# Kernel optimization log

Hardware: AMD Instinct MI355X
Metric: run time of the kernel (lower is better)

The kernel has to match this reference:

```python
import jax, jax.numpy as jnp
import numpy as np
import math

B, T, O, C, H, L, V, S = 4, 1024, 128, 1024, 16, 4, 32000, 4096
D = C // H
PAD = 0


def setup_inputs() -> dict:
    key = jax.random.key(0)
    ks = jax.random.split(key, 16)
    r = lambda i, shape, s=0.02: jax.random.normal(ks[i], shape, jnp.float32) * s
    return {
        "tokens_w": jax.random.randint(ks[0], (B, T), 0, V).astype(jnp.int32),
        "pos_offset": 0,
        "mem": jax.random.normal(ks[1], (B, O, C), jnp.float32),
        "ssum": jax.random.normal(ks[2], (B, C), jnp.float32),
        "tok_emb_w": r(3, (V, C)),
        "pos_emb_w": r(4, (S, C)),
        "mem_w": r(5, (C, C)), "mem_b": jnp.zeros((C,), jnp.float32),
        "memln_s": jnp.ones((C,), jnp.float32), "memln_b": jnp.zeros((C,), jnp.float32),
        "alpha_p": jnp.zeros((C,), jnp.float32),
        "sum_w": r(6, (C, C)),
        "ln1_s": jnp.ones((L, C), jnp.float32), "ln1_b": jnp.zeros((L, C), jnp.float32),
        "Wq": r(7, (L, C, C)), "bq": jnp.zeros((L, C), jnp.float32),
        "Wk": r(8, (L, C, C)), "bk": jnp.zeros((L, C), jnp.float32),
        "Wv": r(9, (L, C, C)), "bv": jnp.zeros((L, C), jnp.float32),
        "Wo": r(10, (L, C, C)), "bo": jnp.zeros((L, C), jnp.float32),
        "ln2_s": jnp.ones((L, C), jnp.float32), "ln2_b": jnp.zeros((L, C), jnp.float32),
        "W1": r(11, (L, C, 4 * C)), "b1": jnp.zeros((L, 4 * C), jnp.float32),
        "W2": r(12, (L, 4 * C, C)), "b2": jnp.zeros((L, C), jnp.float32),
        "fln_s": jnp.ones((C,), jnp.float32), "fln_b": jnp.zeros((C,), jnp.float32),
        "head_w": r(13, (C, V)), "head_b": jnp.zeros((V,), jnp.float32),
        "lam_p": jnp.zeros((C,), jnp.float32),
    }


def _ln(x, s, b, eps=1e-6):
    mu = jnp.mean(x, -1, keepdims=True)
    var = jnp.mean((x - mu) ** 2, -1, keepdims=True)
    return (x - mu) * jax.lax.rsqrt(var + eps) * s + b


def reference(tokens_w, pos_offset, mem, ssum, tok_emb_w, pos_emb_w, mem_w, mem_b,
              memln_s, memln_b, alpha_p, sum_w, ln1_s, ln1_b, Wq, bq, Wk, bk, Wv, bv,
              Wo, bo, ln2_s, ln2_b, W1, b1, W2, b2, fln_s, fln_b, head_w, head_b, lam_p):
    Bx, Tx = tokens_w.shape
    tok = tok_emb_w[tokens_w]                                   # [B,T,C]
    pos_ids = jnp.clip(jnp.arange(Tx, dtype=jnp.int32) + pos_offset, 0, S - 1)
    x = tok + pos_emb_w[pos_ids][None, :, :]
    # memory adapter + norm (saved-before-masking memory state)
    m2 = _ln(mem @ mem_w + mem_b, memln_s, memln_b)             # [B,O,C]
    alpha = jax.nn.sigmoid(alpha_p)
    x = x + ((ssum @ sum_w) * alpha[None, :])[:, None, :]
    # boolean mask: memory tokens always visible + causal window + key padding
    causal = jnp.concatenate([jnp.ones((Tx, O), bool),
                              jnp.tril(jnp.ones((Tx, Tx), bool))], axis=1)[None, None]
    key_ok = jnp.concatenate([jnp.ones((Bx, O), bool), tokens_w != PAD], axis=1)
    mask = causal & key_ok[:, None, None, :]                    # [B,1,T,O+T]
    scale = 1.0 / math.sqrt(D)
    for i in range(L):
        kv = jnp.concatenate([m2, x], axis=1)                   # [B,O+T,C]
        h = _ln(x, ln1_s[i], ln1_b[i])
        q = (h @ Wq[i] + bq[i]).reshape(Bx, Tx, H, D)
        k = (kv @ Wk[i] + bk[i]).reshape(Bx, O + Tx, H, D)
        v = (kv @ Wv[i] + bv[i]).reshape(Bx, O + Tx, H, D)
        att = jnp.einsum('bqhd,bkhd->bhqk', q, k) * scale
        att = jnp.where(mask, att, -1e9)
        p = jax.nn.softmax(att, axis=-1)
        o = jnp.einsum('bhqk,bkhd->bqhd', p, v).reshape(Bx, Tx, C)
        x = x + (o @ Wo[i] + bo[i])
        h = _ln(x, ln2_s[i], ln2_b[i])
        x = x + (jax.nn.gelu(h @ W1[i] + b1[i]) @ W2[i] + b2[i])
    x = _ln(x, fln_s, fln_b)
    new_mem = x[:, -O:, :]
    m = (tokens_w != PAD).astype(x.dtype)
    x = x * m[:, :, None]
    logits = x @ head_w + head_b                                # [B,T,V]
    summary = jnp.sum(x * m[:, :, None], axis=1) / (jnp.sum(m, axis=1, keepdims=True) + 1e-6)
    lam = jax.nn.sigmoid(lam_p)
    new_ssum = ssum * lam[None, :] + summary * (1.0 - lam[None, :])
    return (new_mem, new_ssum, logits)
```

## Files before the change

kernel.cpp:

```cpp
#include <hip/hip_runtime.h>
#include <hip/hip_bf16.h>

typedef __bf16 bf16_t;
typedef __bf16 bf16x8 __attribute__((ext_vector_type(8)));
typedef __bf16 bf16x4 __attribute__((ext_vector_type(4)));
typedef float f32x4 __attribute__((ext_vector_type(4)));

#define NB 4
#define NT 1024
#define NO 128
#define NC 1024
#define NH 16
#define NL 4
#define NV 32000
#define NS 4096
#define ND 64
#define NTK (NO + NT)

#define GLOAD_LDS16(g, l) __builtin_amdgcn_global_load_lds( \
    (__attribute__((address_space(1))) void*)(g), \
    (__attribute__((address_space(3))) void*)(l), 16, 0, 0)

__device__ __forceinline__ float sigmoidf_(float x) { return 1.0f / (1.0f + __expf(-x)); }

#define EPI_F32  0
#define EPI_ADD  1
#define EPI_GELU 2
#define EPI_QKV  3
#define EPI_KV   4

template<int EPI>
__global__ __launch_bounds__(512) void gemm8p(
    const bf16_t* __restrict__ A, const bf16_t* __restrict__ Bt,
    const float* __restrict__ bias, float* __restrict__ outF,
    bf16_t* __restrict__ outB, int M, int N, int K, int ldo, int gm)
{
    __shared__ bf16_t sm[65536];
    const int tid = threadIdx.x;
    const int w = tid >> 6, lane = tid & 63;
    const int wr = w >> 2, wc = w & 3;
    const int lr = lane & 15, lk = lane >> 4;
    const int nwg = gridDim.x;
    const int bid = blockIdx.x;
    const int xcd = bid & 7, base = bid >> 3;
    const int qq = nwg >> 3, rr = nwg & 7;
    int wg = (xcd < rr ? xcd * (qq + 1) : rr * (qq + 1) + (xcd - rr) * qq) + base;
    const int nnt = N >> 8;
    const int gsz = gm * nnt;
    const int g = wg / gsz, r2 = wg - g * gsz;
    const int ntl = r2 / gm, mt = g * gm + (r2 - ntl * gm);
    const int bm = mt << 8, bn = ntl << 8;
    const bf16_t* Ab = A + (size_t)bm * K;
    const bf16_t* Bb = Bt + (size_t)bn * K;
    const int srow = tid >> 3;
    const int scol = ((tid & 7) ^ (srow & 7)) << 3;
    const int nk = K >> 6;
    f32x4 acc[8][4] = {};

    auto STAGE = [&](int b, int kt, int h) {
        const bf16_t* gsrc = (h < 2) ? Ab : Bb;
        const int half = h & 1;
        char* lbase = (char*)(sm + ((h < 2) ? 0 : 32768) + b * 16384 + half * 8192);
        #pragma unroll
        for (int i = 0; i < 2; ++i) {
            GLOAD_LDS16(gsrc + (size_t)(half * 128 + i * 64 + srow) * K + kt * 64 + scol,
                        lbase + (i * 512 + tid) * 16);
        }
    };

    #pragma unroll
    for (int h = 0; h < 4; ++h) STAGE(0, 0, h);
    asm volatile("s_waitcnt vmcnt(0)" ::: "memory");
    __builtin_amdgcn_s_barrier();

    for (int kt = 0; kt < nk; ++kt) {
        const int curb = kt & 1;
        const bool dostage = (kt + 1) < nk;
        const char* Abase = (const char*)(sm + curb * 16384);
        const char* Bbase = (const char*)(sm + 32768 + curb * 16384);

        if (dostage) {
            STAGE(curb ^ 1, kt + 1, 0);
            STAGE(curb ^ 1, kt + 1, 1);
            asm volatile("s_waitcnt vmcnt(4)" ::: "memory");
        } else {
            asm volatile("s_waitcnt vmcnt(0)" ::: "memory");
        }
        __builtin_amdgcn_s_barrier();

        bf16x8 bfr[4][2];
        #pragma unroll
        for (int n = 0; n < 4; ++n)
            #pragma unroll
            for (int ks = 0; ks < 2; ++ks) {
                const int row = wc * 64 + n * 16 + lr;
                bfr[n][ks] = *(const bf16x8*)(Bbase + row * 128 + ((((ks << 2) + lk) ^ (row & 7)) << 4));
            }
        bf16x8 af[4][2];
        #pragma unroll
        for (int m = 0; m < 4; ++m)
            #pragma unroll
            for (int ks = 0; ks < 2; ++ks) {
                const int row = wr * 128 + m * 16 + lr;
                af[m][ks] = *(const bf16x8*)(Abase + row * 128 + ((((ks << 2) + lk) ^ (row & 7)) << 4));
            }
        asm volatile("s_waitcnt lgkmcnt(0)" ::: "memory");
        __builtin_amdgcn_sched_barrier(0);
        __builtin_amdgcn_s_setprio(1);
        #pragma unroll
        for (int m = 0; m < 4; ++m)
            #pragma unroll
            for (int n = 0; n < 4; ++n)
                #pragma unroll
                for (int ks = 0; ks < 2; ++ks)
                    acc[m][n] = __builtin_amdgcn_mfma_f32_16x16x32_bf16(
                        af[m][ks], bfr[n][ks], acc[m][n], 0, 0, 0);
        __builtin_amdgcn_s_setprio(0);

        if (dostage) {
            STAGE(curb ^ 1, kt + 1, 2);
            STAGE(curb ^ 1, kt + 1, 3);
        }
        bf16x8 ag[4][2];
        #pragma unroll
        for (int m = 0; m < 4; ++m)
            #pragma unroll
            for (int ks = 0; ks < 2; ++ks) {
                const int row = wr * 128 + 64 + m * 16 + lr;
                ag[m][ks] = *(const bf16x8*)(Abase + row * 128 + ((((ks << 2) + lk) ^ (row & 7)) << 4));
            }
        asm volatile("s_waitcnt lgkmcnt(0)" ::: "memory");
        __builtin_amdgcn_sched_barrier(0);
        __builtin_amdgcn_s_setprio(1);
        #pragma unroll
        for (int m = 0; m < 4; ++m)
            #pragma unroll
            for (int n = 0; n < 4; ++n)
                #pragma unroll
                for (int ks = 0; ks < 2; ++ks)
                    acc[4 + m][n] = __builtin_amdgcn_mfma_f32_16x16x32_bf16(
                        ag[m][ks], bfr[n][ks], acc[4 + m][n], 0, 0, 0);
        __builtin_amdgcn_s_setprio(0);
        __builtin_amdgcn_s_barrier();
    }

    float bv4[4];
    #pragma unroll
    for (int n = 0; n < 4; ++n) bv4[n] = bias[bn + wc * 64 + n * 16 + lr];
    #pragma unroll
    for (int m = 0; m < 8; ++m) {
        #pragma unroll
        for (int j = 0; j < 4; ++j) {
            const int row = bm + wr * 128 + m * 16 + lk * 4 + j;
            #pragma unroll
            for (int n = 0; n < 4; ++n) {
                const int col = bn + wc * 64 + n * 16 + lr;
                float v = acc[m][n][j] + bv4[n];
                if constexpr (EPI == 0) {
                    __builtin_nontemporal_store(v, &outF[(size_t)row * ldo + col]);
                } else {
                    float u = 1.5957691216057308f * (v + 0.044715f * v * v * v);
                    float g_ = v / (1.0f + __expf(-u));
                    outB[(size_t)row * ldo + col] = (bf16_t)g_;
                }
            }
        }
    }
}

template<int EPI>
__global__ __launch_bounds__(256) void gemm128(
    const bf16_t* __restrict__ A, const bf16_t* __restrict__ Bt,
    const float* __restrict__ bias, const float* __restrict__ bias2,
    float* __restrict__ outF, bf16_t* __restrict__ outB, bf16_t* __restrict__ outB2,
    int M, int N, int K, int p0, int ldo, int gm)
{
    __shared__ bf16_t sm[32768];
    char* smb = (char*)sm;
    const int tid = threadIdx.x;
    const int w = tid >> 6, lane = tid & 63;
    const int wr = w >> 1, wc = w & 1;
    const int lr = lane & 15, lk = lane >> 4;
    const int nwg = gridDim.x;
    const int bid = blockIdx.x;
    const int xcd = bid & 7, base = bid >> 3;
    const int qq = nwg >> 3, rr = nwg & 7;
    int wg = (xcd < rr ? xcd * (qq + 1) : rr * (qq + 1) + (xcd - rr) * qq) + base;
    const int nnt = N >> 7;
    const int gsz = gm * nnt;
    const int g = wg / gsz, r2 = wg - g * gsz;
    const int ntl = r2 / gm, mt = g * gm + (r2 - ntl * gm);
    const int bm = mt << 7, bn = ntl << 7;
    const bf16_t* Ab = A + (size_t)bm * K;
    const bf16_t* Bb = Bt + (size_t)bn * K;
    const int srow = tid >> 3;
    const int scol = ((tid & 7) ^ (srow & 7)) << 3;
    const int nk = K >> 6;
    f32x4 acc[4][4] = {};

    auto STAGE = [&](int b, int kt, int h) {
        const bf16_t* gsrc = h ? Bb : Ab;
        char* lbase = smb + h * 32768 + b * 16384;
        #pragma unroll
        for (int i = 0; i < 4; ++i) {
            GLOAD_LDS16(gsrc + (size_t)(i * 32 + srow) * K + kt * 64 + scol,
                        lbase + (i * 256 + tid) * 16);
        }
    };

    STAGE(0, 0, 0); STAGE(0, 0, 1);
    asm volatile("s_waitcnt vmcnt(0)" ::: "memory");
    __builtin_amdgcn_s_barrier();

    for (int kt = 0; kt < nk; ++kt) {
        const int curb = kt & 1;
        const bool dostage = (kt + 1) < nk;
        const char* Abase = smb + curb * 16384;
        const char* Bbase = smb + 32768 + curb * 16384;

        if (dostage) {
            STAGE(curb ^ 1, kt + 1, 0);
            asm volatile("s_waitcnt vmcnt(4)" ::: "memory");
        } else {
            asm volatile("s_waitcnt vmcnt(0)" ::: "memory");
        }
        __builtin_amdgcn_s_barrier();

        bf16x8 bfr[4][2];
        #pragma unroll
        for (int n = 0; n < 4; ++n)
            #pragma unroll
            for (int ks = 0; ks < 2; ++ks) {
                const int row = wc * 64 + n * 16 + lr;
                bfr[n][ks] = *(const bf16x8*)(Bbase + row * 128 + ((((ks << 2) + lk) ^ (row & 7)) << 4));
            }
        bf16x8 af[4];
        #pragma unroll
        for (int m = 0; m < 4; ++m) {
            const int row = wr * 64 + m * 16 + lr;
            af[m] = *(const bf16x8*)(Abase + row * 128 + (((lk) ^ (row & 7)) << 4));
        }
        asm volatile("s_waitcnt lgkmcnt(0)" ::: "memory");
        __builtin_amdgcn_sched_barrier(0);
        __builtin_amdgcn_s_setprio(1);
        #pragma unroll
        for (int m = 0; m < 4; ++m)
            #pragma unroll
            for (int n = 0; n < 4; ++n)
                acc[m][n] = __builtin_amdgcn_mfma_f32_16x16x32_bf16(
                    af[m], bfr[n][0], acc[m][n], 0, 0, 0);
        __builtin_amdgcn_s_setprio(0);

        if (dostage) STAGE(curb ^ 1, kt + 1, 1);
        bf16x8 ag[4];
        #pragma unroll
        for (int m = 0; m < 4; ++m) {
            const int row = wr * 64 + m * 16 + lr;
            ag[m] = *(const bf16x8*)(Abase + row * 128 + (((4 + lk) ^ (row & 7)) << 4));
        }
        asm volatile("s_waitcnt lgkmcnt(0)" ::: "memory");
        __builtin_amdgcn_sched_barrier(0);
        __builtin_amdgcn_s_setprio(1);
        #pragma unroll
        for (int m = 0; m < 4; ++m)
            #pragma unroll
            for (int n = 0; n < 4; ++n)
                acc[m][n] = __builtin_amdgcn_mfma_f32_16x16x32_bf16(
                    ag[m], bfr[n][1], acc[m][n], 0, 0, 0);
        __builtin_amdgcn_s_setprio(0);
        __builtin_amdgcn_s_barrier();
    }

    #pragma unroll
    for (int m = 0; m < 4; ++m) {
        #pragma unroll
        for (int j = 0; j < 4; ++j) {
            const int row = bm + wr * 64 + m * 16 + lk * 4 + j;
            int b_ = 0, t_ = 0;
            if constexpr (EPI == EPI_QKV || EPI == EPI_KV) { b_ = row / p0; t_ = row % p0; }
            #pragma unroll
            for (int n = 0; n < 4; ++n) {
                const int col = bn + wc * 64 + n * 16 + lr;
                if constexpr (EPI == EPI_F32) {
                    float v = acc[m][n][j] + bias[col];
                    __builtin_nontemporal_store(v, &outF[(size_t)row * ldo + col]);
                } else if constexpr (EPI == EPI_ADD) {
                    float v = acc[m][n][j] + bias[col];
                    outF[(size_t)row * ldo + col] += v;
                } else if constexpr (EPI == EPI_QKV) {
                    float v = acc[m][n][j] + bias[col];
                    int h = col >> 6, d = col & 63;
                    outB[(((size_t)b_ * NH + h) * p0 + t_) * ND + d] = (bf16_t)v;
                } else if constexpr (EPI == EPI_KV) {
                    if (col < NC) {
                        float v = acc[m][n][j] + bias[col];
                        int h = col >> 6, d = col & 63;
                        outB[(((size_t)b_ * NH + h) * NTK + t_) * ND + d] = (bf16_t)v;
                    } else {
                        int c2_ = col - NC;
                        float v = acc[m][n][j] + bias2[c2_];
                        int h = c2_ >> 6, d = c2_ & 63;
                        outB2[(((size_t)b_ * NH + h) * ND + d) * NTK + t_] = (bf16_t)v;
                    }
                }
            }
        }
    }
}

template<int EPI>
__global__ __launch_bounds__(256) void gemm_bt(
    const bf16_t* __restrict__ A, const bf16_t* __restrict__ Bt,
    const float* __restrict__ bias, const float* __restrict__ bias2,
    float* __restrict__ outF, bf16_t* __restrict__ outB, bf16_t* __restrict__ outB2,
    int M, int N, int K, int p0, int ldo, int gm)
{
    __shared__ bf16_t lA[128 * 32];
    __shared__ bf16_t lB[128 * 32];
    const int tid = threadIdx.x;
    const int nwg = gridDim.x;
    const int bid = blockIdx.x;
    const int xcd = bid & 7, base = bid >> 3;
    const int qq = nwg >> 3, rr = nwg & 7;
    int wg = (xcd < rr ? xcd * (qq + 1) : rr * (qq + 1) + (xcd - rr) * qq) + base;
    const int nnt = N >> 7;
    const int gsz = gm * nnt;
    const int g = wg / gsz, r2 = wg - g * gsz;
    const int ntl = r2 / gm, mt = g * gm + (r2 - ntl * gm);
    const int bm = mt * 128, bn = ntl * 128;
    const bf16_t* Ab = A + (size_t)bm * K;
    const bf16_t* Bb = Bt + (size_t)bn * K;
    const int wave = tid >> 6, lane = tid & 63;
    const int wr = wave >> 1, wc = wave & 1;
    const int lr = lane & 15, lk = lane >> 4;
    f32x4 acc[4][4] = {};
    const int nk = K >> 5;
    const int c1 = tid, c2 = tid + 256;
    for (int kt = 0; kt < nk; ++kt) {
        __syncthreads();
        const bf16_t* Abk = Ab + kt * 32;
        const bf16_t* Bbk = Bb + kt * 32;
        GLOAD_LDS16(Abk + (size_t)(c1 >> 2) * K + (c1 & 3) * 8, (char*)lA + c1 * 16);
        GLOAD_LDS16(Abk + (size_t)(c2 >> 2) * K + (c2 & 3) * 8, (char*)lA + c2 * 16);
        GLOAD_LDS16(Bbk + (size_t)(c1 >> 2) * K + (c1 & 3) * 8, (char*)lB + c1 * 16);
        GLOAD_LDS16(Bbk + (size_t)(c2 >> 2) * K + (c2 & 3) * 8, (char*)lB + c2 * 16);
        __syncthreads();
        bf16x8 af[4], bfr[4];
        #pragma unroll
        for (int m = 0; m < 4; ++m)
            af[m] = *(const bf16x8*)&lA[(wr * 64 + m * 16 + lr) * 32 + lk * 8];
        #pragma unroll
        for (int n = 0; n < 4; ++n)
            bfr[n] = *(const bf16x8*)&lB[(wc * 64 + n * 16 + lr) * 32 + lk * 8];
        #pragma unroll
        for (int m = 0; m < 4; ++m)
            #pragma unroll
            for (int n = 0; n < 4; ++n)
                acc[m][n] = __builtin_amdgcn_mfma_f32_16x16x32_bf16(af[m], bfr[n], acc[m][n], 0, 0, 0);
    }
    #pragma unroll
    for (int m = 0; m < 4; ++m) {
        #pragma unroll
        for (int j = 0; j < 4; ++j) {
            const int row = bm + wr * 64 + m * 16 + lk * 4 + j;
            #pragma unroll
            for (int n = 0; n < 4; ++n) {
                const int col = bn + wc * 64 + n * 16 + lr;
                if constexpr (EPI == EPI_F32) {
                    float v = acc[m][n][j] + bias[col];
                    __builtin_nontemporal_store(v, &outF[(size_t)row * ldo + col]);
                }
            }
        }
    }
}

__device__ __forceinline__ void tc_body(
    const float* __restrict__ W, bf16_t* __restrict__ Wt,
    int K, int N, int k0, int n0, int t)
{
    __shared__ float tile[64][65];
    #pragma unroll
    for (int i = 0; i < 4; ++i) {
        const int idx = t + i * 256;
        const int r = idx >> 4, c4 = (idx & 15) << 2;
        const float4 v = *(const float4*)(W + (size_t)(k0 + r) * N + n0 + c4);
        tile[r][c4 + 0] = v.x; tile[r][c4 + 1] = v.y;
        tile[r][c4 + 2] = v.z; tile[r][c4 + 3] = v.w;
    }
    __syncthreads();
    #pragma unroll
    for (int i = 0; i < 4; ++i) {
        const int idx = t + i * 256;
        const int r = idx >> 4, c4 = (idx & 15) << 2;
        bf16x4 o = {(bf16_t)tile[c4 + 0][r], (bf16_t)tile[c4 + 1][r],
                    (bf16_t)tile[c4 + 2][r], (bf16_t)tile[c4 + 3][r]};
        *(bf16x4*)(Wt + (size_t)(n0 + r) * K + k0 + c4) = o;
    }
}

__global__ __launch_bounds__(256) void transpose_cast(
    const float* __restrict__ W, bf16_t* __restrict__ Wt, int K, int N)
{
    tc_body(W, Wt, K, N, blockIdx.x << 6, blockIdx.y << 6, threadIdx.x);
}

__global__ __launch_bounds__(256) void transpose_layer(
    const float* __restrict__ Wq, const float* __restrict__ Wk,
    const float* __restrict__ Wv, const float* __restrict__ Wo,
    const float* __restrict__ W1, const float* __restrict__ W2,
    bf16_t* __restrict__ wtq, bf16_t* __restrict__ wtkv,
    bf16_t* __restrict__ wto, bf16_t* __restrict__ wt1, bf16_t* __restrict__ wt2)
{
    const int bid = blockIdx.x;
    const float* W; bf16_t* Wt; int K, N, k0, n0;
    if (bid < 1024) {
        const int which = bid >> 8, r = bid & 255;
        K = NC; N = NC;
        k0 = (r & 15) << 6; n0 = (r >> 4) << 6;
        W  = (which == 0) ? Wq : (which == 1) ? Wk : (which == 2) ? Wv : Wo;
        Wt = (which == 0) ? wtq : (which == 1) ? wtkv
           : (which == 2) ? (wtkv + (size_t)NC * NC) : wto;
    } else if (bid < 2048) {
        const int r = bid - 1024;
        K = NC; N = 4 * NC;
        k0 = (r & 15) << 6; n0 = (r >> 4) << 6;
        W = W1; Wt = wt1;
    } else {
        const int r = bid - 2048;
        K = 4 * NC; N = NC;
        k0 = (r & 63) << 6; n0 = (r >> 6) << 6;
        W = W2; Wt = wt2;
    }
    tc_body(W, Wt, K, N, k0, n0, threadIdx.x);
}

template<int MODE>
__global__ __launch_bounds__(256) void ln_row(
    const float* __restrict__ X, const float* __restrict__ sw,
    const float* __restrict__ bw, float* __restrict__ outF,
    bf16_t* __restrict__ outB, bf16_t* __restrict__ outB2)
{
    const int row = blockIdx.x;
    const int t = threadIdx.x;
    const float4 v = ((const float4*)(X + (size_t)row * NC))[t];
    float s1 = v.x + v.y + v.z + v.w;
    float s2 = v.x * v.x + v.y * v.y + v.z * v.z + v.w * v.w;
    #pragma unroll
    for (int off = 32; off > 0; off >>= 1) { s1 += __shfl_xor(s1, off); s2 += __shfl_xor(s2, off); }
    __shared__ float rs1[4], rs2[4];
    if ((t & 63) == 0) { rs1[t >> 6] = s1; rs2[t >> 6] = s2; }
    __syncthreads();
    s1 = rs1[0] + rs1[1] + rs1[2] + rs1[3];
    s2 = rs2[0] + rs2[1] + rs2[2] + rs2[3];
    const float mu = s1 * (1.0f / NC);
    const float var = s2 * (1.0f / NC) - mu * mu;
    const float rstd = rsqrtf(var + 1e-6f);
    const int c = t * 4;
    const float4 sv = ((const float4*)sw)[t];
    const float4 bv = ((const float4*)bw)[t];
    float y0 = (v.x - mu) * rstd * sv.x + bv.x;
    float y1 = (v.y - mu) * rstd * sv.y + bv.y;
    float y2 = (v.z - mu) * rstd * sv.z + bv.z;
    float y3 = (v.w - mu) * rstd * sv.w + bv.w;
    size_t dst;
    if constexpr (MODE == 1) dst = ((size_t)(row / NO) * NTK + (row % NO)) * NC + c;
    else dst = (size_t)row * NC + c;
    bf16x4 o = {(bf16_t)y0, (bf16_t)y1, (bf16_t)y2, (bf16_t)y3};
    *(bf16x4*)(outB + dst) = o;
    if constexpr (MODE == 3) {
        const int b_ = row >> 10, t_ = row & 1023;
        bf16x4 o2 = {(bf16_t)v.x, (bf16_t)v.y, (bf16_t)v.z, (bf16_t)v.w};
        *(bf16x4*)(outB2 + ((size_t)b_ * NTK + NO + t_) * NC + c) = o2;
    }
}

__global__ __launch_bounds__(256) void ln_final(
    const float* __restrict__ X, const float* __restrict__ sw,
    const float* __restrict__ bw, const int* __restrict__ tokens,
    bf16_t* __restrict__ xm, float* __restrict__ outMem)
{
    const int row = blockIdx.x;
    const int t = threadIdx.x;
    const float4 v = ((const float4*)(X + (size_t)row * NC))[t];
    float s1 = v.x + v.y + v.z + v.w;
    float s2 = v.x * v.x + v.y * v.y + v.z * v.z + v.w * v.w;
    #pragma unroll
    for (int off = 32; off > 0; off >>= 1) { s1 += __shfl_xor(s1, off); s2 += __shfl_xor(s2, off); }
    __shared__ float rs1[4], rs2[4];
    if ((t & 63) == 0) { rs1[t >> 6] = s1; rs2[t >> 6] = s2; }
    __syncthreads();
    s1 = rs1[0] + rs1[1] + rs1[2] + rs1[3];
    s2 = rs2[0] + rs2[1] + rs2[2] + rs2[3];
    const float mu = s1 * (1.0f / NC);
    const float var = s2 * (1.0f / NC) - mu * mu;
    const float rstd = rsqrtf(var + 1e-6f);
    const int c = t * 4;
    const float4 sv = ((const float4*)sw)[t];
    const float4 bv = ((const float4*)bw)[t];
    float y0 = (v.x - mu) * rstd * sv.x + bv.x;
    float y1 = (v.y - mu) * rstd * sv.y + bv.y;
    float y2 = (v.z - mu) * rstd * sv.z + bv.z;
    float y3 = (v.w - mu) * rstd * sv.w + bv.w;
    const bool ok = tokens[row] != 0;
    bf16x4 o;
    if (ok) { o = (bf16x4){(bf16_t)y0, (bf16_t)y1, (bf16_t)y2, (bf16_t)y3}; }
    else    { o = (bf16x4){(bf16_t)0.f, (bf16_t)0.f, (bf16_t)0.f, (bf16_t)0.f}; }
    *(bf16x4*)(xm + (size_t)row * NC + c) = o;
    const int b_ = row >> 10, t_ = row & 1023;
    if (t_ >= NT - NO) {
        float4 f; f.x = y0; f.y = y1; f.z = y2; f.w = y3;
        *(float4*)(outMem + ((size_t)b_ * NO + (t_ - (NT - NO))) * NC + c) = f;
    }
}

__global__ __launch_bounds__(256) void attn_kernel(
    const bf16_t* __restrict__ Q, const bf16_t* __restrict__ Kb,
    const bf16_t* __restrict__ Vt, const int* __restrict__ tokens,
    bf16_t* __restrict__ Ob)
{
    const int bh = blockIdx.x;
    const int b = bh >> 4, h = bh & 15;
    const int w = threadIdx.x >> 6;
    const int lane = threadIdx.x & 63;
    const int yt = gridDim.y - 1 - blockIdx.y;
    const int q0 = (yt << 7) + (w << 5);
    const int lr = lane & 15, lk = lane >> 4;
    const bf16_t* Qp = Q + ((size_t)bh * NT + q0) * ND;
    bf16x8 qf[2][2];
    #pragma unroll
    for (int qs = 0; qs < 2; ++qs) {
        qf[qs][0] = *(const bf16x8*)(Qp + (qs * 16 + lr) * ND + lk * 8);
        qf[qs][1] = *(const bf16x8*)(Qp + (qs * 16 + lr) * ND + 32 + lk * 8);
    }
    const bf16_t* Kbase = Kb + (size_t)bh * NTK * ND;
    const bf16_t* Vbase = Vt + (size_t)bh * ND * NTK;
    const int* tokb = tokens + b * NT;
    float mrow[2][4] = {{-1e30f, -1e30f, -1e30f, -1e30f}, {-1e30f, -1e30f, -1e30f, -1e30f}};
    float lsum[2][4] = {};
    f32x4 acc[2][4] = {};
    __shared__ bf16_t pb[4][2][16 * 64];
    const int kmax = NO + q0 + 32;
    for (int k0 = 0; k0 < kmax; k0 += 64) {
        f32x4 st[2][4] = {};
        __builtin_amdgcn_s_setprio(1);
        #pragma unroll
        for (int nt = 0; nt < 4; ++nt) {
            const bf16_t* Kp = Kbase + (size_t)(k0 + nt * 16 + lr) * ND + lk * 8;
            bf16x8 kf0 = *(const bf16x8*)(Kp);
            bf16x8 kf1 = *(const bf16x8*)(Kp + 32);
            #pragma unroll
            for (int qs = 0; qs < 2; ++qs) {
                st[qs][nt] = __builtin_amdgcn_mfma_f32_16x16x32_bf16(qf[qs][0], kf0, st[qs][nt], 0, 0, 0);
                st[qs][nt] = __builtin_amdgcn_mfma_f32_16x16x32_bf16(qf[qs][1], kf1, st[qs][nt], 0, 0, 0);
            }
        }
        __builtin_amdgcn_s_setprio(0);
        #pragma unroll
        for (int qs = 0; qs < 2; ++qs) {
            char* pbq = (char*)pb[w][qs];
            float sc[4][4];
            float tmax[4] = {-1e30f, -1e30f, -1e30f, -1e30f};
            #pragma unroll
            for (int nt = 0; nt < 4; ++nt) {
                const int key = k0 + nt * 16 + lr;
                const int kt = key - NO;
                const int kts = kt < 0 ? 0 : kt;
                const bool keyok = (kt < 0) | (tokb[kts] != 0);
                #pragma unroll
                for (int j = 0; j < 4; ++j) {
                    const int qrow = q0 + qs * 16 + lk * 4 + j;
                    const bool ok = keyok && (kt <= qrow);
                    const float s = ok ? st[qs][nt][j] * 0.125f : -1e9f;
                    sc[nt][j] = s;
                    tmax[j] = fmaxf(tmax[j], s);
                }
            }
            #pragma unroll
            for (int off = 1; off < 16; off <<= 1)
                #pragma unroll
                for (int j = 0; j < 4; ++j) tmax[j] = fmaxf(tmax[j], __shfl_xor(tmax[j], off));
            float resc[4], p[4][4], psum[4] = {0.f, 0.f, 0.f, 0.f};
            #pragma unroll
            for (int j = 0; j < 4; ++j) {
                const float mnew = fmaxf(mrow[qs][j], tmax[j]);
                resc[j] = __expf(mrow[qs][j] - mnew);
                mrow[qs][j] = mnew;
            }
            #pragma unroll
            for (int nt = 0; nt < 4; ++nt)
                #pragma unroll
                for (int j = 0; j < 4; ++j) { p[nt][j] = __expf(sc[nt][j] - mrow[qs][j]); psum[j] += p[nt][j]; }
            #pragma unroll
            for (int off = 1; off < 16; off <<= 1)
                #pragma unroll
                for (int j = 0; j < 4; ++j) psum[j] += __shfl_xor(psum[j], off);
            #pragma unroll
            for (int j = 0; j < 4; ++j) lsum[qs][j] = lsum[qs][j] * resc[j] + psum[j];
            #pragma unroll
            for (int dt = 0; dt < 4; ++dt)
                #pragma unroll
                for (int j = 0; j < 4; ++j) acc[qs][dt][j] *= resc[j];
            #pragma unroll
            for (int nt = 0; nt < 4; ++nt)
                #pragma unroll
                for (int j = 0; j < 4; ++j) {
                    const int row = lk * 4 + j;
                    const int byt = (row << 7) + ((((nt << 4) + lr) << 1) ^ ((row & 7) << 4));
                    *(bf16_t*)(pbq + byt) = (bf16_t)p[nt][j];
                }
        }
        const int swz = (lr & 7) << 4;
        bf16x8 pa[2][2];
        #pragma unroll
        for (int qs = 0; qs < 2; ++qs) {
            const char* pbq = (const char*)pb[w][qs];
            pa[qs][0] = *(const bf16x8*)(pbq + ((lr << 7) + (((lk << 4)) ^ swz)));
            pa[qs][1] = *(const bf16x8*)(pbq + ((lr << 7) + ((64 + (lk << 4)) ^ swz)));
        }
        __builtin_amdgcn_s_setprio(1);
        #pragma unroll
        for (int dt = 0; dt < 4; ++dt) {
            const bf16_t* Vp = Vbase + (size_t)(dt * 16 + lr) * NTK + k0 + lk * 8;
            bf16x8 vf0 = *(const bf16x8*)(Vp);
            bf16x8 vf1 = *(const bf16x8*)(Vp + 32);
            #pragma unroll
            for (int qs = 0; qs < 2; ++qs) {
                acc[qs][dt] = __builtin_amdgcn_mfma_f32_16x16x32_bf16(pa[qs][0], vf0, acc[qs][dt], 0, 0, 0);
                acc[qs][dt] = __builtin_amdgcn_mfma_f32_16x16x32_bf16(pa[qs][1], vf1, acc[qs][dt], 0, 0, 0);
            }
        }
        __builtin_amdgcn_s_setprio(0);
    }
    #pragma unroll
    for (int qs = 0; qs < 2; ++qs)
        #pragma unroll
        for (int dt = 0; dt < 4; ++dt)
            #pragma unroll
            for (int j = 0; j < 4; ++j)
                Ob[((size_t)b * NT + q0 + qs * 16 + lk * 4 + j) * NC + h * ND + dt * 16 + lr] =
                    (bf16_t)(acc[qs][dt][j] / lsum[qs][j]);
}

__global__ __launch_bounds__(256) void sum_proj_kernel(
    const float* __restrict__ ssum, const float* __restrict__ sumw,
    const float* __restrict__ alpha, float* __restrict__ add)
{
    const int b = blockIdx.y;
    const int c = blockIdx.x * 256 + threadIdx.x;
    float a = 0.f;
    for (int k = 0; k < NC; ++k) a += ssum[b * NC + k] * sumw[(size_t)k * NC + c];
    add[b * NC + c] = a * sigmoidf_(alpha[c]);
}

__global__ __launch_bounds__(256) void embed_kernel(
    const int* __restrict__ tokens, const int* __restrict__ posoff,
    const float* __restrict__ tokw, const float* __restrict__ posw,
    const float* __restrict__ add, float* __restrict__ X)
{
    const int bt = blockIdx.x;
    const int b = bt >> 10, t = bt & 1023;
    const int c = threadIdx.x * 4;
    const int tok = tokens[bt];
    int p = t + posoff[0];
    p = p < 0 ? 0 : (p > NS - 1 ? NS - 1 : p);
    const float4 tv = *(const float4*)(tokw + (size_t)tok * NC + c);
    const float4 pv = *(const float4*)(posw + (size_t)p * NC + c);
    const float4 av = *(const float4*)(add + b * NC + c);
    float4 o;
    o.x = tv.x + pv.x + av.x; o.y = tv.y + pv.y + av.y;
    o.z = tv.z + pv.z + av.z; o.w = tv.w + pv.w + av.w;
    *(float4*)(X + (size_t)bt * NC + c) = o;
}

__global__ __launch_bounds__(256) void cast_f32_bf16_kernel(
    const float* __restrict__ in, bf16_t* __restrict__ out)
{
    const size_t i = ((size_t)blockIdx.x * 256 + threadIdx.x) * 4;
    const float4 v = *(const float4*)(in + i);
    bf16x4 o = {(bf16_t)v.x, (bf16_t)v.y, (bf16_t)v.z, (bf16_t)v.w};
    *(bf16x4*)(out + i) = o;
}

__global__ __launch_bounds__(256) void sumpart_kernel(
    const bf16_t* __restrict__ XM, float* __restrict__ sbuf)
{
    const int b = blockIdx.z;
    const int c = blockIdx.x * 256 + threadIdx.x;
    const int t0 = blockIdx.y * 64;
    float a = 0.f;
    for (int t = t0; t < t0 + 64; ++t)
        a += (float)XM[((size_t)b * NT + t) * NC + c];
    atomicAdd(&sbuf[b * NC + c], a);
}

__global__ __launch_bounds__(256) void ssum_out_kernel(
    const float* __restrict__ sbuf, const int* __restrict__ tokens,
    const float* __restrict__ ssum, const float* __restrict__ lamp, float* __restrict__ out)
{
    const int b = blockIdx.y;
    const int c = blockIdx.x * 256 + threadIdx.x;
    int cnt = 0;
    for (int t = 0; t < NT; ++t) cnt += (tokens[b * NT + t] != 0);
    const float summary = sbuf[b * NC + c] / ((float)cnt + 1e-6f);
    const float lam = sigmoidf_(lamp[c]);
    out[b * NC + c] = ssum[b * NC + c] * lam + summary * (1.0f - lam);
}

extern "C" void kernel_launch(void* const* d_in, const int* in_sizes, int n_in,
                              void* d_out, int out_size, void* d_ws, size_t ws_size,
                              hipStream_t stream)
{
    (void)in_sizes; (void)n_in; (void)out_size; (void)ws_size;
    const int*   tokens   = (const int*)d_in[0];
    const int*   posoff   = (const int*)d_in[1];
    const float* mem      = (const float*)d_in[2];
    const float* ssum     = (const float*)d_in[3];
    const float* tok_emb  = (const float*)d_in[4];
    const float* pos_emb  = (const float*)d_in[5];
    const float* mem_w    = (const float*)d_in[6];
    const float* mem_b    = (const float*)d_in[7];
    const float* memln_s  = (const float*)d_in[8];
    const float* memln_b  = (const float*)d_in[9];
    const float* alpha_p  = (const float*)d_in[10];
    const float* sum_w    = (const float*)d_in[11];
    const float* ln1_s    = (const float*)d_in[12];
    const float* ln1_b    = (const float*)d_in[13];
    const float* Wq       = (const float*)d_in[14];
    const float* bq       = (const float*)d_in[15];
    const float* Wk       = (const float*)d_in[16];
    const float* bk       = (const float*)d_in[17];
    const float* Wv       = (const float*)d_in[18];
    const float* bv       = (const float*)d_in[19];
    const float* Wo       = (const float*)d_in[20];
    const float* bo       = (const float*)d_in[21];
    const float* ln2_s    = (const float*)d_in[22];
    const float* ln2_b    = (const float*)d_in[23];
    const float* W1       = (const float*)d_in[24];
    const float* b1       = (const float*)d_in[25];
    const float* W2       = (const float*)d_in[26];
    const float* b2       = (const float*)d_in[27];
    const float* fln_s    = (const float*)d_in[28];
    const float* fln_b    = (const float*)d_in[29];
    const float* head_w   = (const float*)d_in[30];
    const float* head_b   = (const float*)d_in[31];
    const float* lam_p    = (const float*)d_in[32];

    float* out_mem    = (float*)d_out;
    float* out_ssum   = out_mem + (size_t)NB * NO * NC;
    float* out_logits = out_ssum + (size_t)NB * NC;

    char* wp = (char*)d_ws;
    auto alloc = [&](size_t bytes) { char* p = wp; wp += (bytes + 255) & ~(size_t)255; return p; };
    bf16_t* wt_head = (bf16_t*)alloc((size_t)NV * NC * 2);
    bf16_t* wt_mem  = (bf16_t*)alloc((size_t)NC * NC * 2);
    bf16_t* wt_q    = (bf16_t*)alloc((size_t)NC * NC * 2);
    bf16_t* wt_kv   = (bf16_t*)alloc((size_t)2 * NC * NC * 2);
    bf16_t* wt_o    = (bf16_t*)alloc((size_t)NC * NC * 2);
    bf16_t* wt_1    = (bf16_t*)alloc((size_t)NC * 4 * NC * 2);
    bf16_t* wt_2    = (bf16_t*)alloc((size_t)NC * 4 * NC * 2);
    float*  xbuf    = (float*)alloc((size_t)NB * NT * NC * 4);
    bf16_t* hbuf    = (bf16_t*)alloc((size_t)NB * NT * NC * 2);
    bf16_t* kvbuf   = (bf16_t*)alloc((size_t)NB * NTK * NC * 2);
    bf16_t* qbuf    = (bf16_t*)alloc((size_t)NB * NT * NC * 2);
    bf16_t* kbuf    = (bf16_t*)alloc((size_t)NB * NTK * NC * 2);
    bf16_t* vtbuf   = (bf16_t*)alloc((size_t)NB * NTK * NC * 2);
    bf16_t* obuf    = (bf16_t*)alloc((size_t)NB * NT * NC * 2);
    bf16_t* midbuf  = (bf16_t*)alloc((size_t)NB * NT * 4 * NC * 2);
    bf16_t* xmbuf   = (bf16_t*)alloc((size_t)NB * NT * NC * 2);
    bf16_t* membf   = (bf16_t*)alloc((size_t)NB * NO * NC * 2);
    float*  m2f     = (float*)alloc((size_t)NB * NO * NC * 4);
    float*  addb    = (float*)alloc((size_t)NB * NC * 4);
    float*  sbuf    = (float*)alloc((size_t)NB * NC * 4);

    hipMemsetAsync(sbuf, 0, (size_t)NB * NC * 4, stream);

    transpose_cast<<<dim3(NC / 64, NV / 64), 256, 0, stream>>>(head_w, wt_head, NC, NV);
    transpose_cast<<<dim3(NC / 64, NC / 64), 256, 0, stream>>>(mem_w, wt_mem, NC, NC);

    cast_f32_bf16_kernel<<<(NB * NO * NC) / 1024, 256, 0, stream>>>(mem, membf);
    gemm_bt<EPI_F32><<<32, 256, 0, stream>>>(
        membf, wt_mem, mem_b, nullptr, m2f, nullptr, nullptr, NB * NO, NC, NC, 0, NC, 4);
    ln_row<1><<<NB * NO, 256, 0, stream>>>(m2f, memln_s, memln_b, nullptr, kvbuf, nullptr);

    sum_proj_kernel<<<dim3(NC / 256, NB), 256, 0, stream>>>(ssum, sum_w, alpha_p, addb);
    embed_kernel<<<NB * NT, 256, 0, stream>>>(tokens, posoff, tok_emb, pos_emb, addb, xbuf);

    for (int i = 0; i < NL; ++i) {
        transpose_layer<<<3072, 256, 0, stream>>>(
            Wq + (size_t)i * NC * NC, Wk + (size_t)i * NC * NC,
            Wv + (size_t)i * NC * NC, Wo + (size_t)i * NC * NC,
            W1 + (size_t)i * NC * 4 * NC, W2 + (size_t)i * 4 * NC * NC,
            wt_q, wt_kv, wt_o, wt_1, wt_2);

        ln_row<3><<<NB * NT, 256, 0, stream>>>(xbuf, ln1_s + i * NC, ln1_b + i * NC, nullptr, hbuf, kvbuf);

        gemm128<EPI_QKV><<<256, 256, 0, stream>>>(
            hbuf, wt_q, bq + i * NC, nullptr, nullptr, qbuf, nullptr, NB * NT, NC, NC, NT, 0, 8);
        gemm128<EPI_KV><<<576, 256, 0, stream>>>(
            kvbuf, wt_kv, bk + i * NC, bv + i * NC, nullptr, kbuf, vtbuf, NB * NTK, 2 * NC, NC, NTK, 0, 6);

        attn_kernel<<<dim3(NB * NH, NT / 128), 256, 0, stream>>>(qbuf, kbuf, vtbuf, tokens, obuf);

        gemm128<EPI_ADD><<<256, 256, 0, stream>>>(
            obuf, wt_o, bo + i * NC, nullptr, xbuf, nullptr, nullptr, NB * NT, NC, NC, 0, NC, 8);

        ln_row<0><<<NB * NT, 256, 0, stream>>>(xbuf, ln2_s + i * NC, ln2_b + i * NC, nullptr, hbuf, nullptr);
        gemm8p<1><<<256, 512, 0, stream>>>(
            hbuf, wt_1, b1 + (size_t)i * 4 * NC, nullptr, midbuf, NB * NT, 4 * NC, NC, 4 * NC, 4);
        gemm128<EPI_ADD><<<256, 256, 0, stream>>>(
            midbuf, wt_2, b2 + i * NC, nullptr, xbuf, nullptr, nullptr, NB * NT, NC, 4 * NC, 0, NC, 2);
    }

    ln_final<<<NB * NT, 256, 0, stream>>>(xbuf, fln_s, fln_b, tokens, xmbuf, out_mem);
    sumpart_kernel<<<dim3(NC / 256, NT / 64, NB), 256, 0, stream>>>(xmbuf, sbuf);
    ssum_out_kernel<<<dim3(NC / 256, NB), 256, 0, stream>>>(sbuf, tokens, ssum, lam_p, out_ssum);
    gemm8p<0><<<2000, 512, 0, stream>>>(
        xmbuf, wt_head, head_b, out_logits, nullptr, NB * NT, NV, NC, NV, 4);
}
```

Measured before the change: 1.723 ms.

## Replace 256x256 GEMM with 128-tile GEMM and split-K for FFN down-projection

Removes the 512-thread 256x256-tile GEMM and runs the FFN up-projection (with fused GELU) and the vocab head on the 128x128-tile kernel, which launches many more workgroups. The FFN down-projection (K=4096) is split two ways along K, each half writing fp32 partial sums, and a new elementwise kernel adds both partials, the bias and the residual. The aim is better occupancy and wave balance across compute units. The cost is lower per-tile data reuse, more global traffic for the partial buffers, and an extra launch.

```diff
diff --git a/kernel.cpp b/kernel.cpp
--- a/kernel.cpp
+++ b/kernel.cpp
@@ -28,152 +28,14 @@
 #define EPI_GELU 2
 #define EPI_QKV  3
 #define EPI_KV   4
-
-template<int EPI>
-__global__ __launch_bounds__(512) void gemm8p(
-    const bf16_t* __restrict__ A, const bf16_t* __restrict__ Bt,
-    const float* __restrict__ bias, float* __restrict__ outF,
-    bf16_t* __restrict__ outB, int M, int N, int K, int ldo, int gm)
-{
-    __shared__ bf16_t sm[65536];
-    const int tid = threadIdx.x;
-    const int w = tid >> 6, lane = tid & 63;
-    const int wr = w >> 2, wc = w & 3;
-    const int lr = lane & 15, lk = lane >> 4;
-    const int nwg = gridDim.x;
-    const int bid = blockIdx.x;
-    const int xcd = bid & 7, base = bid >> 3;
-    const int qq = nwg >> 3, rr = nwg & 7;
-    int wg = (xcd < rr ? xcd * (qq + 1) : rr * (qq + 1) + (xcd - rr) * qq) + base;
-    const int nnt = N >> 8;
-    const int gsz = gm * nnt;
-    const int g = wg / gsz, r2 = wg - g * gsz;
-    const int ntl = r2 / gm, mt = g * gm + (r2 - ntl * gm);
-    const int bm = mt << 8, bn = ntl << 8;
-    const bf16_t* Ab = A + (size_t)bm * K;
-    const bf16_t* Bb = Bt + (size_t)bn * K;
-    const int srow = tid >> 3;
-    const int scol = ((tid & 7) ^ (srow & 7)) << 3;
-    const int nk = K >> 6;
-    f32x4 acc[8][4] = {};
-
-    auto STAGE = [&](int b, int kt, int h) {
-        const bf16_t* gsrc = (h < 2) ? Ab : Bb;
-        const int half = h & 1;
-        char* lbase = (char*)(sm + ((h < 2) ? 0 : 32768) + b * 16384 + half * 8192);
-        #pragma unroll
-        for (int i = 0; i < 2; ++i) {
-            GLOAD_LDS16(gsrc + (size_t)(half * 128 + i * 64 + srow) * K + kt * 64 + scol,
-                        lbase + (i * 512 + tid) * 16);
-        }
-    };
-
-    #pragma unroll
-    for (int h = 0; h < 4; ++h) STAGE(0, 0, h);
-    asm volatile("s_waitcnt vmcnt(0)" ::: "memory");
-    __builtin_amdgcn_s_barrier();
-
-    for (int kt = 0; kt < nk; ++kt) {
-        const int curb = kt & 1;
-        const bool dostage = (kt + 1) < nk;
-        const char* Abase = (const char*)(sm + curb * 16384);
-        const char* Bbase = (const char*)(sm + 32768 + curb * 16384);
-
-        if (dostage) {
-            STAGE(curb ^ 1, kt + 1, 0);
-            STAGE(curb ^ 1, kt + 1, 1);
-            asm volatile("s_waitcnt vmcnt(4)" ::: "memory");
-        } else {
-            asm volatile("s_waitcnt vmcnt(0)" ::: "memory");
-        }
-        __builtin_amdgcn_s_barrier();
-
-        bf16x8 bfr[4][2];
-        #pragma unroll
-        for (int n = 0; n < 4; ++n)
-            #pragma unroll
-            for (int ks = 0; ks < 2; ++ks) {
-                const int row = wc * 64 + n * 16 + lr;
-                bfr[n][ks] = *(const bf16x8*)(Bbase + row * 128 + ((((ks << 2) + lk) ^ (row & 7)) << 4));
-            }
-        bf16x8 af[4][2];
-        #pragma unroll
-        for (int m = 0; m < 4; ++m)
-            #pragma unroll
-            for (int ks = 0; ks < 2; ++ks) {
-                const int row = wr * 128 + m * 16 + lr;
-                af[m][ks] = *(const bf16x8*)(Abase + row * 128 + ((((ks << 2) + lk) ^ (row & 7)) << 4));
-            }
-        asm volatile("s_waitcnt lgkmcnt(0)" ::: "memory");
-        __builtin_amdgcn_sched_barrier(0);
-        __builtin_amdgcn_s_setprio(1);
-        #pragma unroll
-        for (int m = 0; m < 4; ++m)
-            #pragma unroll
-            for (int n = 0; n < 4; ++n)
-                #pragma unroll
-                for (int ks = 0; ks < 2; ++ks)
-                    acc[m][n] = __builtin_amdgcn_mfma_f32_16x16x32_bf16(
-                        af[m][ks], bfr[n][ks], acc[m][n], 0, 0, 0);
-        __builtin_amdgcn_s_setprio(0);
-
-        if (dostage) {
-            STAGE(curb ^ 1, kt + 1, 2);
-            STAGE(curb ^ 1, kt + 1, 3);
-        }
-        bf16x8 ag[4][2];
-        #pragma unroll
-        for (int m = 0; m < 4; ++m)
-            #pragma unroll
-            for (int ks = 0; ks < 2; ++ks) {
-                const int row = wr * 128 + 64 + m * 16 + lr;
-                ag[m][ks] = *(const bf16x8*)(Abase + row * 128 + ((((ks << 2) + lk) ^ (row & 7)) << 4));
-            }
-        asm volatile("s_waitcnt lgkmcnt(0)" ::: "memory");
-        __builtin_amdgcn_sched_barrier(0);
-        __builtin_amdgcn_s_setprio(1);
-        #pragma unroll
-        for (int m = 0; m < 4; ++m)
-            #pragma unroll
-            for (int n = 0; n < 4; ++n)
-                #pragma unroll
-                for (int ks = 0; ks < 2; ++ks)
-                    acc[4 + m][n] = __builtin_amdgcn_mfma_f32_16x16x32_bf16(
-                        ag[m][ks], bfr[n][ks], acc[4 + m][n], 0, 0, 0);
-        __builtin_amdgcn_s_setprio(0);
-        __builtin_amdgcn_s_barrier();
-    }
-
-    float bv4[4];
-    #pragma unroll
-    for (int n = 0; n < 4; ++n) bv4[n] = bias[bn + wc * 64 + n * 16 + lr];
-    #pragma unroll
-    for (int m = 0; m < 8; ++m) {
-        #pragma unroll
-        for (int j = 0; j < 4; ++j) {
-            const int row = bm + wr * 128 + m * 16 + lk * 4 + j;
-            #pragma unroll
-            for (int n = 0; n < 4; ++n) {
-                const int col = bn + wc * 64 + n * 16 + lr;
-                float v = acc[m][n][j] + bv4[n];
-                if constexpr (EPI == 0) {
-                    __builtin_nontemporal_store(v, &outF[(size_t)row * ldo + col]);
-                } else {
-                    float u = 1.5957691216057308f * (v + 0.044715f * v * v * v);
-                    float g_ = v / (1.0f + __expf(-u));
-                    outB[(size_t)row * ldo + col] = (bf16_t)g_;
-                }
-            }
-        }
-    }
-}
+#define EPI_PART 5
 
 template<int EPI>
 __global__ __launch_bounds__(256) void gemm128(
     const bf16_t* __restrict__ A, const bf16_t* __restrict__ Bt,
     const float* __restrict__ bias, const float* __restrict__ bias2,
     float* __restrict__ outF, bf16_t* __restrict__ outB, bf16_t* __restrict__ outB2,
-    int M, int N, int K, int p0, int ldo, int gm)
+    int M, int N, int K, int p0, int ldo, int gm, int ks)
 {
     __shared__ bf16_t sm[32768];
     char* smb = (char*)sm;
@@ -187,15 +49,18 @@
     const int qq = nwg >> 3, rr = nwg & 7;
     int wg = (xcd < rr ? xcd * (qq + 1) : rr * (qq + 1) + (xcd - rr) * qq) + base;
     const int nnt = N >> 7;
+    const int tiles = (M >> 7) * nnt;
+    const int ksl = wg / tiles; wg -= ksl * tiles;
     const int gsz = gm * nnt;
     const int g = wg / gsz, r2 = wg - g * gsz;
     const int ntl = r2 / gm, mt = g * gm + (r2 - ntl * gm);
     const int bm = mt << 7, bn = ntl << 7;
-    const bf16_t* Ab = A + (size_t)bm * K;
-    const bf16_t* Bb = Bt + (size_t)bn * K;
+    const int Ksl = K / ks;
+    const bf16_t* Ab = A + (size_t)bm * K + ksl * Ksl;
+    const bf16_t* Bb = Bt + (size_t)bn * K + ksl * Ksl;
     const int srow = tid >> 3;
     const int scol = ((tid & 7) ^ (srow & 7)) << 3;
-    const int nk = K >> 6;
+    const int nk = Ksl >> 6;
     f32x4 acc[4][4] = {};
 
     auto STAGE = [&](int b, int kt, int h) {
@@ -230,9 +95,9 @@
         #pragma unroll
         for (int n = 0; n < 4; ++n)
             #pragma unroll
-            for (int ks = 0; ks < 2; ++ks) {
+            for (int ks_ = 0; ks_ < 2; ++ks_) {
                 const int row = wc * 64 + n * 16 + lr;
-                bfr[n][ks] = *(const bf16x8*)(Bbase + row * 128 + ((((ks << 2) + lk) ^ (row & 7)) << 4));
+                bfr[n][ks_] = *(const bf16x8*)(Bbase + row * 128 + ((((ks_ << 2) + lk) ^ (row & 7)) << 4));
             }
         bf16x8 af[4];
         #pragma unroll
@@ -271,6 +136,8 @@
         __builtin_amdgcn_s_barrier();
     }
 
+    float* outP = outF;
+    if constexpr (EPI == EPI_PART) outP = outF + (size_t)ksl * M * ldo;
     #pragma unroll
     for (int m = 0; m < 4; ++m) {
         #pragma unroll
@@ -284,9 +151,16 @@
                 if constexpr (EPI == EPI_F32) {
                     float v = acc[m][n][j] + bias[col];
                     __builtin_nontemporal_store(v, &outF[(size_t)row * ldo + col]);
+                } else if constexpr (EPI == EPI_PART) {
+                    __builtin_nontemporal_store(acc[m][n][j], &outP[(size_t)row * ldo + col]);
                 } else if constexpr (EPI == EPI_ADD) {
                     float v = acc[m][n][j] + bias[col];
                     outF[(size_t)row * ldo + col] += v;
+                } else if constexpr (EPI == EPI_GELU) {
+                    float v = acc[m][n][j] + bias[col];
+                    float u = 1.5957691216057308f * (v + 0.044715f * v * v * v);
+                    float g_ = v / (1.0f + __expf(-u));
+                    outB[(size_t)row * ldo + col] = (bf16_t)g_;
                 } else if constexpr (EPI == EPI_QKV) {
                     float v = acc[m][n][j] + bias[col];
                     int h = col >> 6, d = col & 63;
@@ -306,6 +180,22 @@
             }
         }
     }
+}
+
+__global__ __launch_bounds__(256) void ffn2_reduce(
+    const float* __restrict__ p, const float* __restrict__ b2,
+    float* __restrict__ xbuf)
+{
+    const size_t i = ((size_t)blockIdx.x * 256 + threadIdx.x) * 4;
+    const int c = (int)(i & (NC - 1));
+    const float4 x = *(const float4*)(xbuf + i);
+    const float4 a = *(const float4*)(p + i);
+    const float4 b = *(const float4*)(p + (size_t)NB * NT * NC + i);
+    const float4 bb = *(const float4*)(b2 + c);
+    float4 o;
+    o.x = x.x + a.x + b.x + bb.x; o.y = x.y + a.y + b.y + bb.y;
+    o.z = x.z + a.z + b.z + bb.z; o.w = x.w + a.w + b.w + bb.w;
+    *(float4*)(xbuf + i) = o;
 }
 
 template<int EPI>
@@ -770,6 +660,7 @@
     bf16_t* xmbuf   = (bf16_t*)alloc((size_t)NB * NT * NC * 2);
     bf16_t* membf   = (bf16_t*)alloc((size_t)NB * NO * NC * 2);
     float*  m2f     = (float*)alloc((size_t)NB * NO * NC * 4);
+    float*  pbuf    = (float*)alloc((size_t)2 * NB * NT * NC * 4);
     float*  addb    = (float*)alloc((size_t)NB * NC * 4);
     float*  sbuf    = (float*)alloc((size_t)NB * NC * 4);
 
@@ -796,25 +687,29 @@
         ln_row<3><<<NB * NT, 256, 0, stream>>>(xbuf, ln1_s + i * NC, ln1_b + i * NC, nullptr, hbuf, kvbuf);
 
         gemm128<EPI_QKV><<<256, 256, 0, stream>>>(
-            hbuf, wt_q, bq + i * NC, nullptr, nullptr, qbuf, nullptr, NB * NT, NC, NC, NT, 0, 8);
+            hbuf, wt_q, bq + i * NC, nullptr, nullptr, qbuf, nullptr, NB * NT, NC, NC, NT, 0, 8, 1);
         gemm128<EPI_KV><<<576, 256, 0, stream>>>(
-            kvbuf, wt_kv, bk + i * NC, bv + i * NC, nullptr, kbuf, vtbuf, NB * NTK, 2 * NC, NC, NTK, 0, 6);
+            kvbuf, wt_kv, bk + i * NC, bv + i * NC, nullptr, kbuf, vtbuf, NB * NTK, 2 * NC, NC, NTK, 0, 6, 1);
 
         attn_kernel<<<dim3(NB * NH, NT / 128), 256, 0, stream>>>(qbuf, kbuf, vtbuf, tokens, obuf);
 
         gemm128<EPI_ADD><<<256, 256, 0, stream>>>(
-            obuf, wt_o, bo + i * NC, nullptr, xbuf, nullptr, nullptr, NB * NT, NC, NC, 0, NC, 8);
+            obuf, wt_o, bo + i * NC, nullptr, xbuf, nullptr, nullptr, NB * NT, NC, NC, 0, NC, 8, 1);
 
         ln_row<0><<<NB * NT, 256, 0, stream>>>(xbuf, ln2_s + i * NC, ln2_b + i * NC, nullptr, hbuf, nullptr);
-        gemm8p<1><<<256, 512, 0, stream>>>(
-            hbuf, wt_1, b1 + (size_t)i * 4 * NC, nullptr, midbuf, NB * NT, 4 * NC, NC, 4 * NC, 4);
-        gemm128<EPI_ADD><<<256, 256, 0, stream>>>(
-            midbuf, wt_2, b2 + i * NC, nullptr, xbuf, nullptr, nullptr, NB * NT, NC, 4 * NC, 0, NC, 2);
+        gemm128<EPI_GELU><<<1024, 256, 0, stream>>>(
+            hbuf, wt_1, b1 + (size_t)i * 4 * NC, nullptr, nullptr, midbuf, nullptr,
+            NB * NT, 4 * NC, NC, 0, 4 * NC, 8, 1);
+        gemm128<EPI_PART><<<512, 256, 0, stream>>>(
+            midbuf, wt_2, nullptr, nullptr, pbuf, nullptr, nullptr,
+            NB * NT, NC, 4 * NC, 0, NC, 8, 2);
+        ffn2_reduce<<<(NB * NT * NC) / 1024, 256, 0, stream>>>(pbuf, b2 + i * NC, xbuf);
     }
 
     ln_final<<<NB * NT, 256, 0, stream>>>(xbuf, fln_s, fln_b, tokens, xmbuf, out_mem);
     sumpart_kernel<<<dim3(NC / 256, NT / 64, NB), 256, 0, stream>>>(xmbuf, sbuf);
     ssum_out_kernel<<<dim3(NC / 256, NB), 256, 0, stream>>>(sbuf, tokens, ssum, lam_p, out_ssum);
-    gemm8p<0><<<2000, 512, 0, stream>>>(
-        xmbuf, wt_head, head_b, out_logits, nullptr, NB * NT, NV, NC, NV, 4);
-}
+    gemm128<EPI_F32><<<8000, 256, 0, stream>>>(
+        xmbuf, wt_head, head_b, nullptr, out_logits, nullptr, nullptr,
+        NB * NT, NV, NC, 0, NV, 8, 1);
+}
```

Result: slower. 1.793 ms (+4.1%).

## Split-K the FFN down-projection GEMM with a separate reduce kernel

Applied to the files above, without the earlier changes.

Adds a K-split option to the 128x128 GEMM and runs the FFN2 GEMM (K=4096) as two K-halves over 512 workgroups instead of 256. Each half writes fp32 partials, and a new elementwise kernel adds both partials, the bias and the residual into xbuf. The aim is better occupancy across the CUs, since 256 tiles may underfill the GPU. The cost is an extra 32MB of partial writes and reads plus one more kernel launch per layer. An unused GELU epilogue is also added to gemm128.

```diff
diff --git a/kernel.cpp b/kernel.cpp
--- a/kernel.cpp
+++ b/kernel.cpp
@@ -28,6 +28,7 @@
 #define EPI_GELU 2
 #define EPI_QKV  3
 #define EPI_KV   4
+#define EPI_PART 5
 
 template<int EPI>
 __global__ __launch_bounds__(512) void gemm8p(
@@ -173,7 +174,7 @@
     const bf16_t* __restrict__ A, const bf16_t* __restrict__ Bt,
     const float* __restrict__ bias, const float* __restrict__ bias2,
     float* __restrict__ outF, bf16_t* __restrict__ outB, bf16_t* __restrict__ outB2,
-    int M, int N, int K, int p0, int ldo, int gm)
+    int M, int N, int K, int p0, int ldo, int gm, int ks)
 {
     __shared__ bf16_t sm[32768];
     char* smb = (char*)sm;
@@ -187,15 +188,18 @@
     const int qq = nwg >> 3, rr = nwg & 7;
     int wg = (xcd < rr ? xcd * (qq + 1) : rr * (qq + 1) + (xcd - rr) * qq) + base;
     const int nnt = N >> 7;
+    const int tiles = (M >> 7) * nnt;
+    const int ksl = wg / tiles; wg -= ksl * tiles;
     const int gsz = gm * nnt;
     const int g = wg / gsz, r2 = wg - g * gsz;
     const int ntl = r2 / gm, mt = g * gm + (r2 - ntl * gm);
     const int bm = mt << 7, bn = ntl << 7;
-    const bf16_t* Ab = A + (size_t)bm * K;
-    const bf16_t* Bb = Bt + (size_t)bn * K;
+    const int Ksl = K / ks;
+    const bf16_t* Ab = A + (size_t)bm * K + ksl * Ksl;
+    const bf16_t* Bb = Bt + (size_t)bn * K + ksl * Ksl;
     const int srow = tid >> 3;
     const int scol = ((tid & 7) ^ (srow & 7)) << 3;
-    const int nk = K >> 6;
+    const int nk = Ksl >> 6;
     f32x4 acc[4][4] = {};
 
     auto STAGE = [&](int b, int kt, int h) {
@@ -230,9 +234,9 @@
         #pragma unroll
         for (int n = 0; n < 4; ++n)
             #pragma unroll
-            for (int ks = 0; ks < 2; ++ks) {
+            for (int ks_ = 0; ks_ < 2; ++ks_) {
                 const int row = wc * 64 + n * 16 + lr;
-                bfr[n][ks] = *(const bf16x8*)(Bbase + row * 128 + ((((ks << 2) + lk) ^ (row & 7)) << 4));
+                bfr[n][ks_] = *(const bf16x8*)(Bbase + row * 128 + ((((ks_ << 2) + lk) ^ (row & 7)) << 4));
             }
         bf16x8 af[4];
         #pragma unroll
@@ -271,6 +275,8 @@
         __builtin_amdgcn_s_barrier();
     }
 
+    float* outP = outF;
+    if constexpr (EPI == EPI_PART) outP = outF + (size_t)ksl * M * ldo;
     #pragma unroll
     for (int m = 0; m < 4; ++m) {
         #pragma unroll
@@ -284,9 +290,16 @@
                 if constexpr (EPI == EPI_F32) {
                     float v = acc[m][n][j] + bias[col];
                     __builtin_nontemporal_store(v, &outF[(size_t)row * ldo + col]);
+                } else if constexpr (EPI == EPI_PART) {
+                    __builtin_nontemporal_store(acc[m][n][j], &outP[(size_t)row * ldo + col]);
                 } else if constexpr (EPI == EPI_ADD) {
                     float v = acc[m][n][j] + bias[col];
                     outF[(size_t)row * ldo + col] += v;
+                } else if constexpr (EPI == EPI_GELU) {
+                    float v = acc[m][n][j] + bias[col];
+                    float u = 1.5957691216057308f * (v + 0.044715f * v * v * v);
+                    float g_ = v / (1.0f + __expf(-u));
+                    outB[(size_t)row * ldo + col] = (bf16_t)g_;
                 } else if constexpr (EPI == EPI_QKV) {
                     float v = acc[m][n][j] + bias[col];
                     int h = col >> 6, d = col & 63;
@@ -306,6 +319,22 @@
             }
         }
     }
+}
+
+__global__ __launch_bounds__(256) void ffn2_reduce(
+    const float* __restrict__ p, const float* __restrict__ b2,
+    float* __restrict__ xbuf)
+{
+    const size_t i = ((size_t)blockIdx.x * 256 + threadIdx.x) * 4;
+    const int c = (int)(i & (NC - 1));
+    const float4 x = *(const float4*)(xbuf + i);
+    const float4 a = *(const float4*)(p + i);
+    const float4 b = *(const float4*)(p + (size_t)NB * NT * NC + i);
+    const float4 bb = *(const float4*)(b2 + c);
+    float4 o;
+    o.x = x.x + a.x + b.x + bb.x; o.y = x.y + a.y + b.y + bb.y;
+    o.z = x.z + a.z + b.z + bb.z; o.w = x.w + a.w + b.w + bb.w;
+    *(float4*)(xbuf + i) = o;
 }
 
 template<int EPI>
@@ -770,6 +799,7 @@
     bf16_t* xmbuf   = (bf16_t*)alloc((size_t)NB * NT * NC * 2);
     bf16_t* membf   = (bf16_t*)alloc((size_t)NB * NO * NC * 2);
     float*  m2f     = (float*)alloc((size_t)NB * NO * NC * 4);
+    float*  pbuf    = (float*)alloc((size_t)2 * NB * NT * NC * 4);
     float*  addb    = (float*)alloc((size_t)NB * NC * 4);
     float*  sbuf    = (float*)alloc((size_t)NB * NC * 4);
 
@@ -796,20 +826,22 @@
         ln_row<3><<<NB * NT, 256, 0, stream>>>(xbuf, ln1_s + i * NC, ln1_b + i * NC, nullptr, hbuf, kvbuf);
 
         gemm128<EPI_QKV><<<256, 256, 0, stream>>>(
-            hbuf, wt_q, bq + i * NC, nullptr, nullptr, qbuf, nullptr, NB * NT, NC, NC, NT, 0, 8);
+            hbuf, wt_q, bq + i * NC, nullptr, nullptr, qbuf, nullptr, NB * NT, NC, NC, NT, 0, 8, 1);
         gemm128<EPI_KV><<<576, 256, 0, stream>>>(
-            kvbuf, wt_kv, bk + i * NC, bv + i * NC, nullptr, kbuf, vtbuf, NB * NTK, 2 * NC, NC, NTK, 0, 6);
+            kvbuf, wt_kv, bk + i * NC, bv + i * NC, nullptr, kbuf, vtbuf, NB * NTK, 2 * NC, NC, NTK, 0, 6, 1);
 
         attn_kernel<<<dim3(NB * NH, NT / 128), 256, 0, stream>>>(qbuf, kbuf, vtbuf, tokens, obuf);
 
         gemm128<EPI_ADD><<<256, 256, 0, stream>>>(
-            obuf, wt_o, bo + i * NC, nullptr, xbuf, nullptr, nullptr, NB * NT, NC, NC, 0, NC, 8);
+            obuf, wt_o, bo + i * NC, nullptr, xbuf, nullptr, nullptr, NB * NT, NC, NC, 0, NC, 8, 1);
 
         ln_row<0><<<NB * NT, 256, 0, stream>>>(xbuf, ln2_s + i * NC, ln2_b + i * NC, nullptr, hbuf, nullptr);
         gemm8p<1><<<256, 512, 0, stream>>>(
             hbuf, wt_1, b1 + (size_t)i * 4 * NC, nullptr, midbuf, NB * NT, 4 * NC, NC, 4 * NC, 4);
-        gemm128<EPI_ADD><<<256, 256, 0, stream>>>(
-            midbuf, wt_2, b2 + i * NC, nullptr, xbuf, nullptr, nullptr, NB * NT, NC, 4 * NC, 0, NC, 2);
+        gemm128<EPI_PART><<<512, 256, 0, stream>>>(
+            midbuf, wt_2, nullptr, nullptr, pbuf, nullptr, nullptr,
+            NB * NT, NC, 4 * NC, 0, NC, 8, 2);
+        ffn2_reduce<<<(NB * NT * NC) / 1024, 256, 0, stream>>>(pbuf, b2 + i * NC, xbuf);
     }
 
     ln_final<<<NB * NT, 256, 0, stream>>>(xbuf, fln_s, fln_b, tokens, xmbuf, out_mem);
```

Result: no change. 1.728 ms (+0.3%).
